# Optimization experiments

Measured on AMD Instinct MI355X. Metric: run time of the kernel, lower is better.

## Reference

```python
import jax, jax.numpy as jnp
import numpy as np

LATENT = 256
HEADS = 4
DIM_HEAD = 256            # dim_head = latent_channels
INNER = HEADS * DIM_HEAD  # 1024
ROT_DIM = DIM_HEAD // 2   # rotary dim per coordinate (relative_emb_dim=2)
MIN_FREQ = 1.0 / 64.0     # 1/res
ROT_SCALE = 16.0          # CrossFormer scale
FF_SCALE = 0.5            # Gaussian Fourier feature scale
PI = 3.141592653589793
OUT_CH = 3


def _gelu(x):
    return jax.nn.gelu(x, approximate=False)  # torch nn.GELU default (erf)


def _rot_freqs(coords, dim):
    # coords: [b, n] -> freqs [b, n, dim]
    inv_freq = 1.0 / (10000.0 ** (jnp.arange(0, dim, 2, dtype=jnp.float32) / dim))
    t = coords * (ROT_SCALE / MIN_FREQ)
    f = t[..., None] * inv_freq               # [b, n, dim//2]
    return jnp.concatenate([f, f], axis=-1)    # [b, n, dim]


def _rotate_half(x):
    x1, x2 = jnp.split(x, 2, axis=-1)
    return jnp.concatenate([-x2, x1], axis=-1)


def _apply_rot(t, freqs):
    return t * jnp.cos(freqs) + _rotate_half(t) * jnp.sin(freqs)


def _apply_2d_rot(t, fx, fy):
    d = t.shape[-1]
    tx, ty = t[..., : d // 2], t[..., d // 2 :]
    return jnp.concatenate([_apply_rot(tx, fx), _apply_rot(ty, fy)], axis=-1)


def _inst_norm(t, eps=1e-5):
    # galerkin normalization: non-affine norm over head dim (InstanceNorm1d, affine=False)
    mu = jnp.mean(t, axis=-1, keepdims=True)
    var = jnp.var(t, axis=-1, keepdims=True)
    return (t - mu) * jax.lax.rsqrt(var + eps)


def setup_inputs() -> dict:
    key = jax.random.key(0)
    ks = jax.random.split(key, 20)
    b, nq, nc = 8, 4096, 4096
    s = 0.02
    return {
        "z": jax.random.normal(ks[0], (b, nc, LATENT), jnp.float32),
        "query_pos": jax.random.uniform(ks[1], (b, nq, 2), jnp.float32),
        "context_pos": jax.random.uniform(ks[2], (b, nc, 2), jnp.float32),
        # GaussianFourierFeatureTransform buffer B: [2, mapping_size=latent/2]
        "B_ff": jax.random.normal(ks[3], (2, LATENT // 2), jnp.float32) * FF_SCALE,
        # coordinate_projection linears (bias=False)
        "Wc1": jax.random.normal(ks[4], (LATENT, LATENT), jnp.float32) * s,
        "Wc2": jax.random.normal(ks[5], (LATENT, LATENT), jnp.float32) * s,
        # cross attention projections
        "Wq": jax.random.normal(ks[6], (LATENT, INNER), jnp.float32) * s,
        "Wkv": jax.random.normal(ks[7], (LATENT, 2 * INNER), jnp.float32) * s,
        "Wo": jax.random.normal(ks[8], (INNER, LATENT), jnp.float32) * s,
        "bo": jnp.zeros((LATENT,), jnp.float32),
        # feed-forward (mlp_dim = latent)
        "Wf1": jax.random.normal(ks[9], (LATENT, LATENT), jnp.float32) * s,
        "bf1": jnp.zeros((LATENT,), jnp.float32),
        "Wf2": jax.random.normal(ks[10], (LATENT, LATENT), jnp.float32) * s,
        "bf2": jnp.zeros((LATENT,), jnp.float32),
        # output head
        "Wh1": jax.random.normal(ks[11], (LATENT + 2, LATENT), jnp.float32) * s,
        "Wh2": jax.random.normal(ks[12], (LATENT, LATENT // 2), jnp.float32) * s,
        "Wh3": jax.random.normal(ks[13], (LATENT // 2, OUT_CH), jnp.float32) * s,
        "bh3": jnp.zeros((OUT_CH,), jnp.float32),
    }


def reference(z, query_pos, context_pos, B_ff, Wc1, Wc2, Wq, Wkv, Wo, bo,
              Wf1, bf1, Wf2, bf2, Wh1, Wh2, Wh3, bh3):
    b, nq, _ = query_pos.shape
    nc = z.shape[1]
    # 1) Gaussian Fourier features + 2-layer projection
    ff = 2.0 * PI * (query_pos @ B_ff)                           # [b, nq, latent/2]
    x = jnp.concatenate([jnp.sin(ff), jnp.cos(ff)], axis=-1)      # [b, nq, latent]
    x = _gelu(x @ Wc1) @ Wc2
    # 2) galerkin cross attention with 2D rotary relative pos emb
    q = (x @ Wq).reshape(b, nq, HEADS, DIM_HEAD).transpose(0, 2, 1, 3)
    k, v = jnp.split(z @ Wkv, 2, axis=-1)
    k = k.reshape(b, nc, HEADS, DIM_HEAD).transpose(0, 2, 1, 3)
    v = v.reshape(b, nc, HEADS, DIM_HEAD).transpose(0, 2, 1, 3)
    fxq = _rot_freqs(query_pos[..., 0], ROT_DIM)[:, None]         # [b,1,nq,rot]
    fyq = _rot_freqs(query_pos[..., 1], ROT_DIM)[:, None]
    fxk = _rot_freqs(context_pos[..., 0], ROT_DIM)[:, None]
    fyk = _rot_freqs(context_pos[..., 1], ROT_DIM)[:, None]
    q = _apply_2d_rot(q, fxq, fyq)
    k = _apply_2d_rot(k, fxk, fyk)
    k = _inst_norm(k)
    v = _inst_norm(v)
    kv = jnp.einsum('bhnd,bhne->bhde', k, v)                      # [b,h,d,d]
    attn = jnp.einsum('bhmd,bhde->bhme', q, kv) * (1.0 / nc)      # [b,h,nq,d]
    attn = attn.transpose(0, 2, 1, 3).reshape(b, nq, INNER)
    x = (attn @ Wo + bo) + x                                      # residual
    x = (_gelu(x @ Wf1 + bf1) @ Wf2 + bf2) + x                    # FFN residual
    # 3) output head on [features, coords]
    h = jnp.concatenate([x, query_pos], axis=-1)
    h = _gelu(h @ Wh1)
    h = _gelu(h @ Wh2)
    return h @ Wh3 + bh3                                          # [b, nq, out_ch]
```

## Files before the change

### kernel.cpp

```cpp
#include <hip/hip_runtime.h>
#include <math.h>


typedef unsigned short u16;
typedef __attribute__((ext_vector_type(4))) float f32x4;
typedef __attribute__((ext_vector_type(8))) short s16x8;
typedef __attribute__((ext_vector_type(8))) unsigned short u16x8;
typedef __attribute__((ext_vector_type(4))) unsigned short u16x4;

#define LOG2_1E4_D64 0.20762050593046013f

#define VMCNT(n) do{ asm volatile("s_waitcnt vmcnt(" #n ")" ::: "memory"); \
                     __builtin_amdgcn_sched_barrier(0); }while(0)
#define BARRIER() do{ __builtin_amdgcn_s_barrier(); \
                      __builtin_amdgcn_sched_barrier(0); }while(0)

__device__ __forceinline__ u16 f2b(float f){
  union { float f; unsigned u; } v; v.f = f;
  unsigned u = v.u;
  u += 0x7FFFu + ((u >> 16) & 1u);
  return (u16)(u >> 16);
}
__device__ __forceinline__ float b2f(u16 b){
  union { unsigned u; float f; } v; v.u = ((unsigned)b) << 16; return v.f;
}
__device__ __forceinline__ float gelu_f(float x){
  return 0.5f * x * (1.0f + erff(x * 0.7071067811865475f));
}

#if __has_builtin(__builtin_amdgcn_global_load_lds)
#define HAVE_GLL 1
typedef const __attribute__((address_space(1))) void* as1cv;
typedef __attribute__((address_space(3))) void* as3v;
__device__ __forceinline__ void gload16(const void* g, void* l){
  __builtin_amdgcn_global_load_lds((as1cv)g, (as3v)l, 16, 0, 0);
}
#else
#define HAVE_GLL 0
#endif


struct PrepArgs {
  const float* z; u16* Zb;
  const float* qp; const float* Bff; u16* X0;
  const float* W[9]; u16* Wt[9];
  int K[9]; int N[9]; int boff[10];
  int castB, tcB;
};
__global__ __launch_bounds__(256) void k_prep(PrepArgs a){
  int b = blockIdx.x, tid = threadIdx.x;
  if (b < a.castB){
    long i = (long)b * 256 + tid;
    float4 f = ((const float4*)a.z)[i];
    u16x4 o = { f2b(f.x), f2b(f.y), f2b(f.z), f2b(f.w) };
    ((u16x4*)a.Zb)[i] = o;
  } else if (b < a.castB + a.tcB){
    int bb = b - a.castB;
    int w = 0;
    while (bb >= a.boff[w+1]) w++;
    int idx = (bb - a.boff[w]) * 256 + tid;
    int K = a.K[w], N = a.N[w];
    int n = idx / K, k = idx - n * K;
    a.Wt[w][idx] = f2b(a.W[w][(long)k * N + n]);
  } else {
    int bb = b - a.castB - a.tcB;
    long r = (long)bb * 2 + (tid >> 7);
    int j = tid & 127;
    float qx = a.qp[r*2], qy = a.qp[r*2+1];
    float ff = 6.283185307179586f * (qx * a.Bff[j] + qy * a.Bff[128 + j]);
    a.X0[r*256 + j]       = f2b(sinf(ff));
    a.X0[r*256 + 128 + j] = f2b(cosf(ff));
  }
}

__global__ __launch_bounds__(256) void k_red(const float* __restrict__ p, u16* __restrict__ out, long stride){
  long i = (long)blockIdx.x * 256 + threadIdx.x;
  f32x4 s = ((const f32x4*)p)[i];
  s += ((const f32x4*)(p + stride))[i];
  s += ((const f32x4*)(p + 2*stride))[i];
  s += ((const f32x4*)(p + 3*stride))[i];
  u16x4 o = { f2b(s[0]), f2b(s[1]), f2b(s[2]), f2b(s[3]) };
  ((u16x4*)out)[i] = o;
}

__global__ __launch_bounds__(256) void k_final(const u16* __restrict__ H2, const float* __restrict__ Wh3,
                                               const float* __restrict__ bh3, float* __restrict__ out){
  long r = (long)blockIdx.x * 256 + threadIdx.x;
  float a0 = bh3[0], a1 = bh3[1], a2 = bh3[2];
  const u16x8* hrow = (const u16x8*)(H2 + r*128);
#pragma unroll
  for (int c8 = 0; c8 < 16; c8++){
    u16x8 hv = hrow[c8];
#pragma unroll
    for (int e = 0; e < 8; e++){
      float f = b2f(hv[e]);
      int k = c8*8 + e;
      a0 += f * Wh3[k*3];
      a1 += f * Wh3[k*3+1];
      a2 += f * Wh3[k*3+2];
    }
  }
  out[r*3] = a0; out[r*3+1] = a1; out[r*3+2] = a2;
}


template<int MODE>
__global__ __launch_bounds__(256, 2)
void gemm_fuse(const u16* __restrict__ A, const u16* __restrict__ Bw,
               u16* __restrict__ outK, u16* __restrict__ outV,
               const float* __restrict__ pos){
  __shared__ char smem[49152];
  u16* AsB = (u16*)smem;
  u16* BsB = (u16*)(smem + 16384);

  int tid  = threadIdx.x;
  int lane = tid & 63;
  int wave = tid >> 6;
  int wm = (wave & 1) << 6;
  int wn = (wave >> 1) << 7;
  int whalf = wave >> 1;
  int yb = blockIdx.x;
  int h  = yb & 3;
  bool isK = (MODE == 1) || (yb < 4);
  long m0 = (long)blockIdx.y * 128;

  int r15 = lane & 15;
  int cc  = lane >> 4;
  int fsw = (cc ^ ((r15 >> 1) & 3)) * 8;
  const u16* Bh = Bw + (long)yb * 65536;

  f32x4 acc[4][8];
#pragma unroll
  for (int i = 0; i < 4; i++)
#pragma unroll
    for (int j = 0; j < 8; j++)
      acc[i][j] = f32x4{0.f, 0.f, 0.f, 0.f};

#if HAVE_GLL
  int srow  = lane >> 2;
  int scolS = ((lane & 3) ^ ((lane >> 3) & 3)) * 8;
  int aRow[2], bRow[4];
  const u16 *gA[2], *gB[4];
#pragma unroll
  for (int t = 0; t < 2; t++){
    aRow[t] = (wave*2 + t) * 16;
    gA[t] = A + (m0 + aRow[t] + srow) * 256 + scolS;
  }
#pragma unroll
  for (int t = 0; t < 4; t++){
    bRow[t] = (wave*4 + t) * 16;
    gB[t] = Bh + (bRow[t] + srow) * 256 + scolS;
  }
  auto stage = [&](int buf, int kk){
    u16* ab = AsB + buf*4096;
    u16* bb = BsB + buf*8192;
#pragma unroll
    for (int t = 0; t < 2; t++) gload16(gA[t] + kk*32, ab + aRow[t]*32);
#pragma unroll
    for (int t = 0; t < 4; t++) gload16(gB[t] + kk*32, bb + bRow[t]*32);
  };
  auto compute = [&](int buf){
    const u16* ab = AsB + buf*4096;
    const u16* bb = BsB + buf*8192;
    s16x8 af[4], bf[8];
#pragma unroll
    for (int i = 0; i < 4; i++) af[i] = *(const s16x8*)&ab[(wm + i*16 + r15)*32 + fsw];
#pragma unroll
    for (int j = 0; j < 8; j++) bf[j] = *(const s16x8*)&bb[(wn + j*16 + r15)*32 + fsw];
#pragma unroll
    for (int i = 0; i < 4; i++)
#pragma unroll
      for (int j = 0; j < 8; j++)
        acc[i][j] = __builtin_amdgcn_mfma_f32_16x16x32_bf16(af[i], bf[j], acc[i][j], 0, 0, 0);
  };

  stage(0, 0);
  stage(1, 1);
  int cur = 0;
  for (int t = 0; t < 7; t++){
    VMCNT(6);
    BARRIER();
    compute(cur);
    __builtin_amdgcn_sched_barrier(0);
    BARRIER();
    if (t + 2 < 8) stage(cur, t + 2);
    cur ^= 1;
  }
  VMCNT(0);
  BARRIER();
  compute(cur);
#else
  int sm = tid >> 2, sc = tid & 3;
  for (int k0 = 0; k0 < 256; k0 += 32){
    u16x8 va  = *(const u16x8*)(A + (m0 + sm)*256 + sc*8 + k0);
    u16x8 va1 = *(const u16x8*)(A + (m0 + sm + 64)*256 + sc*8 + k0);
    u16x8 vb0 = *(const u16x8*)(Bh + (sm      )*256 + sc*8 + k0);
    u16x8 vb1 = *(const u16x8*)(Bh + (sm + 64 )*256 + sc*8 + k0);
    u16x8 vb2 = *(const u16x8*)(Bh + (sm + 128)*256 + sc*8 + k0);
    u16x8 vb3 = *(const u16x8*)(Bh + (sm + 192)*256 + sc*8 + k0);
    __syncthreads();
    *(u16x8*)&AsB[sm*32 + sc*8] = va;
    *(u16x8*)&AsB[(sm+64)*32 + sc*8] = va1;
    *(u16x8*)&BsB[sm*32 + sc*8] = vb0;
    *(u16x8*)&BsB[(sm+64)*32 + sc*8] = vb1;
    *(u16x8*)&BsB[(sm+128)*32 + sc*8] = vb2;
    *(u16x8*)&BsB[(sm+192)*32 + sc*8] = vb3;
    __syncthreads();
    s16x8 af[4], bf[8];
#pragma unroll
    for (int i = 0; i < 4; i++) af[i] = *(const s16x8*)&AsB[(wm + i*16 + r15)*32 + cc*8];
#pragma unroll
    for (int j = 0; j < 8; j++) bf[j] = *(const s16x8*)&BsB[(wn + j*16 + r15)*32 + cc*8];
#pragma unroll
    for (int i = 0; i < 4; i++)
#pragma unroll
      for (int j = 0; j < 8; j++)
        acc[i][j] = __builtin_amdgcn_mfma_f32_16x16x32_bf16(af[i], bf[j], acc[i][j], 0, 0, 0);
    __syncthreads();
  }
#endif

  if (isK){
    float invf4[4];
#pragma unroll
    for (int jl = 0; jl < 4; jl++)
      invf4[jl] = 1024.0f * exp2f(-(float)(jl*16 + r15) * LOG2_1E4_D64);
#pragma unroll
    for (int i = 0; i < 4; i++){
#pragma unroll
      for (int r = 0; r < 4; r++){
        long n = m0 + wm + i*16 + cc*4 + r;
        float p = pos[n*2 + whalf];
#pragma unroll
        for (int jl = 0; jl < 4; jl++){
          float a = p * invf4[jl];
          float s = __sinf(a), c = __cosf(a);
          float t0 = acc[i][jl][r], t1 = acc[i][jl+4][r];
          acc[i][jl][r]   = t0*c - t1*s;
          acc[i][jl+4][r] = t1*c + t0*s;
        }
      }
    }
  }

  if constexpr (MODE == 1){
#pragma unroll
    for (int i = 0; i < 4; i++)
#pragma unroll
      for (int j = 0; j < 8; j++)
#pragma unroll
        for (int r = 0; r < 4; r++){
          long row = m0 + wm + i*16 + cc*4 + r;
          int col = yb*256 + wn + j*16 + r15;
          outK[row*1024 + col] = f2b(acc[i][j][r]);
        }
  } else {
    u16*   TB  = (u16*)smem;
    float* PS1 = (float*)(smem + 32768);
    float* PS2 = (float*)(smem + 33792);

    __syncthreads();

#pragma unroll
    for (int i = 0; i < 4; i++){
#pragma unroll
      for (int r = 0; r < 4; r++){
        float s1 = 0.f, s2 = 0.f;
#pragma unroll
        for (int j = 0; j < 8; j++){
          float v = acc[i][j][r];
          s1 += v; s2 += v*v;
        }
#pragma unroll
        for (int m = 1; m < 16; m <<= 1){
          s1 += __shfl_xor(s1, m, 64);
          s2 += __shfl_xor(s2, m, 64);
        }
        int rowid = (wave&1)*64 + i*16 + cc*4 + r;
        if (r15 == 0){ PS1[whalf*128 + rowid] = s1; PS2[whalf*128 + rowid] = s2; }
      }
    }
    __syncthreads();
#pragma unroll
    for (int i = 0; i < 4; i++){
#pragma unroll
      for (int r = 0; r < 4; r++){
        int rowid = (wave&1)*64 + i*16 + cc*4 + r;
        float s1 = PS1[rowid] + PS1[128 + rowid];
        float s2 = PS2[rowid] + PS2[128 + rowid];
        float mu  = s1 * 0.00390625f;
        float var = s2 * 0.00390625f - mu*mu;
        float inv = 1.0f / sqrtf(var + 1e-5f);
#pragma unroll
        for (int j = 0; j < 8; j++)
          acc[i][j][r] = (acc[i][j][r] - mu) * inv;
      }
    }
    __syncthreads();

    u16* outp = isK ? outK : outV;
    int bb  = (int)(m0 >> 12);
    int nn0 = (int)(m0 & 4095);
    long matbase = ((long)(bb*4 + h) * 256) * 4096;
#pragma unroll
    for (int p = 0; p < 2; p++){
      if ((wave & 1) == p){
#pragma unroll
        for (int i = 0; i < 4; i++)
#pragma unroll
          for (int j = 0; j < 8; j++)
#pragma unroll
            for (int r = 0; r < 4; r++){
              int nl = i*16 + cc*4 + r;
              int d  = wn + j*16 + r15;
              TB[nl*256 + (d ^ ((nl>>2)<<1))] = f2b(acc[i][j][r]);
            }
      }
      __syncthreads();
      {
        int n4 = (lane & 15) * 4;
        int sw = (lane & 15) << 1;
#pragma unroll
        for (int rnd = 0; rnd < 16; rnd++){
          int d = rnd*16 + wave*4 + (lane >> 4);
          u16x4 vv;
#pragma unroll
          for (int jj = 0; jj < 4; jj++) vv[jj] = TB[(n4+jj)*256 + (d ^ sw)];
          *(u16x4*)(outp + matbase + (long)d*4096 + nn0 + p*64 + n4) = vv;
        }
      }
      __syncthreads();
    }
  }
}


enum { EP_B = 0, EP_GELU = 1, EP_BIAS_GELU = 2, EP_BIAS_RESB = 3, EP_SCALE = 4,
       EP_QP_GELU = 5, EP_F32 = 6 };

struct GArgs {
  const u16* A; const u16* B;
  u16* Cb; float* Cf;
  const float* bias; const u16* res; const float* qp; const float* wtail;
  float scale;
  int M, N, K, lda, ldb, ldc, NLO;
  long sAh, sAl, sBh, sBl, sCh, sCl;
};

template<int EP>
__global__ __launch_bounds__(256, 2)
void gemm_k(GArgs g){
  int z = blockIdx.z;
  int zh = z / g.NLO, zl = z - zh * g.NLO;
  const u16* A = g.A + (long)zh * g.sAh + (long)zl * g.sAl;
  const u16* B = g.B + (long)zh * g.sBh + (long)zl * g.sBl;
  long coff = (long)zh * g.sCh + (long)zl * g.sCl;

  __shared__ u16 As[2][128*32];
  __shared__ u16 Bs[2][128*32];

  int tid  = threadIdx.x;
  int lane = tid & 63;
  int wave = tid >> 6;
  int wm = (wave & 1) << 6;
  int wn = (wave >> 1) << 6;
  long m0 = (long)blockIdx.x * 128;
  long n0 = (long)blockIdx.y * 128;

  int r15 = lane & 15;
  int cc  = lane >> 4;
  int fsw = (cc ^ ((r15 >> 1) & 3)) * 8;

  f32x4 acc[4][4];
#pragma unroll
  for (int i = 0; i < 4; i++)
#pragma unroll
    for (int j = 0; j < 4; j++)
      acc[i][j] = f32x4{0.f, 0.f, 0.f, 0.f};

#if HAVE_GLL
  int srow  = lane >> 2;
  int scolS = ((lane & 3) ^ ((lane >> 3) & 3)) * 8;
  int aRow[2];
  const u16 *gA[2], *gB[2];
#pragma unroll
  for (int t = 0; t < 2; t++){
    aRow[t] = (wave*2 + t) * 16;
    gA[t] = A + (m0 + aRow[t] + srow) * g.lda + scolS;
    gB[t] = B + (n0 + aRow[t] + srow) * g.ldb + scolS;
  }
  auto stage = [&](int buf, int kk){
#pragma unroll
    for (int t = 0; t < 2; t++){
      gload16(gA[t] + kk*32, &As[buf][aRow[t]*32]);
      gload16(gB[t] + kk*32, &Bs[buf][aRow[t]*32]);
    }
  };
  auto compute = [&](int buf){
    s16x8 af[4], bf[4];
#pragma unroll
    for (int i = 0; i < 4; i++) af[i] = *(const s16x8*)&As[buf][(wm + i*16 + r15)*32 + fsw];
#pragma unroll
    for (int i = 0; i < 4; i++) bf[i] = *(const s16x8*)&Bs[buf][(wn + i*16 + r15)*32 + fsw];
#pragma unroll
    for (int i = 0; i < 4; i++)
#pragma unroll
      for (int j = 0; j < 4; j++)
        acc[i][j] = __builtin_amdgcn_mfma_f32_16x16x32_bf16(af[i], bf[j], acc[i][j], 0, 0, 0);
  };

  int nt = g.K >> 5;
  stage(0, 0);
  stage(1, 1);
  int cur = 0;
  for (int t = 0; t < nt - 1; t++){
    VMCNT(4);
    BARRIER();
    compute(cur);
    __builtin_amdgcn_sched_barrier(0);
    BARRIER();
    if (t + 2 < nt) stage(cur, t + 2);
    cur ^= 1;
  }
  VMCNT(0);
  BARRIER();
  compute(cur);
#else
  int sm  = tid >> 2;
  int sc  = tid & 3;
  for (int k0 = 0; k0 < g.K; k0 += 32){
    u16x8 va0 = *(const u16x8*)(A + (m0 + sm )*g.lda + sc*8 + k0);
    u16x8 va1 = *(const u16x8*)(A + (m0 + sm + 64)*g.lda + sc*8 + k0);
    u16x8 vb0 = *(const u16x8*)(B + (n0 + sm )*g.ldb + sc*8 + k0);
    u16x8 vb1 = *(const u16x8*)(B + (n0 + sm + 64)*g.ldb + sc*8 + k0);
    __syncthreads();
    *(u16x8*)&As[0][sm*32 + sc*8] = va0;
    *(u16x8*)&As[0][(sm+64)*32 + sc*8] = va1;
    *(u16x8*)&Bs[0][sm*32 + sc*8] = vb0;
    *(u16x8*)&Bs[0][(sm+64)*32 + sc*8] = vb1;
    __syncthreads();
    s16x8 af[4], bf[4];
#pragma unroll
    for (int i = 0; i < 4; i++) af[i] = *(const s16x8*)&As[0][(wm + i*16 + r15)*32 + cc*8];
#pragma unroll
    for (int i = 0; i < 4; i++) bf[i] = *(const s16x8*)&Bs[0][(wn + i*16 + r15)*32 + cc*8];
#pragma unroll
    for (int i = 0; i < 4; i++)
#pragma unroll
      for (int j = 0; j < 4; j++)
        acc[i][j] = __builtin_amdgcn_mfma_f32_16x16x32_bf16(af[i], bf[j], acc[i][j], 0, 0, 0);
    __syncthreads();
  }
#endif

  int colb = (int)n0 + wn + r15;
  int rowb = (int)m0 + wm + cc * 4;
#pragma unroll
  for (int i = 0; i < 4; i++){
#pragma unroll
    for (int j = 0; j < 4; j++){
      int col = colb + j*16;
#pragma unroll
      for (int r = 0; r < 4; r++){
        int row = rowb + i*16 + r;
        float v = acc[i][j][r];
        if constexpr (EP == EP_B){
          g.Cb[coff + (long)row * g.ldc + col] = f2b(v);
        } else if constexpr (EP == EP_GELU){
          g.Cb[coff + (long)row * g.ldc + col] = f2b(gelu_f(v));
        } else if constexpr (EP == EP_BIAS_GELU){
          v = gelu_f(v + g.bias[col]);
          g.Cb[coff + (long)row * g.ldc + col] = f2b(v);
        } else if constexpr (EP == EP_BIAS_RESB){
          v += g.bias[col] + b2f(g.res[(long)row * g.ldc + col]);
          g.Cb[coff + (long)row * g.ldc + col] = f2b(v);
        } else if constexpr (EP == EP_SCALE){
          g.Cb[coff + (long)row * g.ldc + col] = f2b(v * g.scale);
        } else if constexpr (EP == EP_F32){
          g.Cf[coff + (long)row * g.ldc + col] = v;
        } else {
          v += g.qp[(long)row*2] * g.wtail[col] + g.qp[(long)row*2+1] * g.wtail[256+col];
          g.Cb[coff + (long)row * g.ldc + col] = f2b(gelu_f(v));
        }
      }
    }
  }
}


extern "C" void kernel_launch(void* const* d_in, const int* in_sizes, int n_in,
                              void* d_out, int out_size, void* d_ws, size_t ws_size,
                              hipStream_t stream){
  const float* z   = (const float*)d_in[0];
  const float* qp  = (const float*)d_in[1];
  const float* cp  = (const float*)d_in[2];
  const float* Bff = (const float*)d_in[3];
  const float* Wc1 = (const float*)d_in[4];
  const float* Wc2 = (const float*)d_in[5];
  const float* Wq  = (const float*)d_in[6];
  const float* Wkv = (const float*)d_in[7];
  const float* Wo  = (const float*)d_in[8];
  const float* bo  = (const float*)d_in[9];
  const float* Wf1 = (const float*)d_in[10];
  const float* bf1 = (const float*)d_in[11];
  const float* Wf2 = (const float*)d_in[12];
  const float* bf2 = (const float*)d_in[13];
  const float* Wh1 = (const float*)d_in[14];
  const float* Wh2 = (const float*)d_in[15];
  const float* Wh3 = (const float*)d_in[16];
  const float* bh3 = (const float*)d_in[17];
  float* out = (float*)d_out;
  (void)in_sizes; (void)n_in; (void)out_size;

  size_t mb = ws_size >> 20;
  int C;
  if      (mb >= 264) C = 1;
  else if (mb >= 168) C = 2;
  else if (mb >= 120) C = 4;
  else                C = 8;
  const int NB = 8 / C;
  const long R = (long)NB * 4096;

  char* ws = (char*)d_ws;
  const size_t MB = 1024*1024;
  u16* WqT  = (u16*)(ws + 0);
  u16* WkvT = (u16*)(ws + 512*1024);
  u16* WoT  = (u16*)(ws + 1536*1024);
  u16* Wc1T = (u16*)(ws + 2048*1024);
  u16* Wc2T = (u16*)(ws + (2048+128)*1024);
  u16* Wf1T = (u16*)(ws + (2048+256)*1024);
  u16* Wf2T = (u16*)(ws + (2048+384)*1024);
  u16* Wh1T = (u16*)(ws + (2048+512)*1024);
  u16* Wh2T = (u16*)(ws + (2048+640)*1024);
  u16* R1 = (u16*)(ws + 4*MB);
  u16* R2 = (u16*)(ws + 20*MB);
  u16* R3 = (u16*)(ws + 36*MB);
  u16* R4 = (u16*)(ws + 52*MB);
  u16* kvT = (u16*)(ws + 68*MB);
  u16* BIG1 = (u16*)(ws + 72*MB);
  u16* BIG2 = (u16*)((char*)BIG1 + (size_t)NB*8*MB);
  u16* BIG3 = (u16*)((char*)BIG2 + (size_t)NB*8*MB);

  u16* X0b = R1; u16* X2b = R1;
  u16* Tb  = R2; u16* H1b = R2;
  u16* Xb  = R3;
  u16* Zb  = R4; u16* H2b = R4;

  auto G = [&](int ep, const u16* A, const u16* B, u16* Cb, float* Cf,
               const float* bias, const u16* res, const float* qq, const float* wtail,
               float scale, int M, int N, int K, int lda, int ldb, int ldc,
               int nz, int NLO, long sAh, long sAl, long sBh, long sBl, long sCh, long sCl){
    GArgs g;
    g.A=A; g.B=B; g.Cb=Cb; g.Cf=Cf; g.bias=bias; g.res=res; g.qp=qq; g.wtail=wtail;
    g.scale=scale; g.M=M; g.N=N; g.K=K; g.lda=lda; g.ldb=ldb; g.ldc=ldc; g.NLO=NLO;
    g.sAh=sAh; g.sAl=sAl; g.sBh=sBh; g.sBl=sBl; g.sCh=sCh; g.sCl=sCl;
    dim3 gr(M/128, N/128, nz); dim3 bl(256);
    switch(ep){
      case EP_B:          gemm_k<EP_B><<<gr,bl,0,stream>>>(g); break;
      case EP_GELU:       gemm_k<EP_GELU><<<gr,bl,0,stream>>>(g); break;
      case EP_BIAS_GELU:  gemm_k<EP_BIAS_GELU><<<gr,bl,0,stream>>>(g); break;
      case EP_BIAS_RESB:  gemm_k<EP_BIAS_RESB><<<gr,bl,0,stream>>>(g); break;
      case EP_SCALE:      gemm_k<EP_SCALE><<<gr,bl,0,stream>>>(g); break;
      case EP_QP_GELU:    gemm_k<EP_QP_GELU><<<gr,bl,0,stream>>>(g); break;
      case EP_F32:        gemm_k<EP_F32><<<gr,bl,0,stream>>>(g); break;
    }
  };

  {
    PrepArgs a;
    a.z = z; a.Zb = Zb; a.qp = qp; a.Bff = Bff; a.X0 = X0b;
    const float* Ws[9] = { Wq, Wkv, Wo, Wc1, Wc2, Wf1, Wf2, Wh1, Wh2 };
    u16* Wts[9] = { WqT, WkvT, WoT, Wc1T, Wc2T, Wf1T, Wf2T, Wh1T, Wh2T };
    int Ks[9] = { 256, 256, 1024, 256, 256, 256, 256, 256, 256 };
    int Ns[9] = { 1024, 2048, 256, 256, 256, 256, 256, 256, 128 };
    int off = 0;
    for (int i = 0; i < 9; i++){
      a.W[i] = Ws[i]; a.Wt[i] = Wts[i]; a.K[i] = Ks[i]; a.N[i] = Ns[i];
      a.boff[i] = off; off += Ks[i]*Ns[i]/256;
    }
    a.boff[9] = off;
    a.castB = 8192; a.tcB = off;
    k_prep<<<dim3(8192 + off + 16384), dim3(256), 0, stream>>>(a);
  }

  G(EP_GELU, X0b, Wc1T, Tb, 0, 0,0,0,0, 1.f, 32768,256,256, 256,256,256, 1,1, 0,0,0,0,0,0);
  G(EP_B,    Tb,  Wc2T, Xb, 0, 0,0,0,0, 1.f, 32768,256,256, 256,256,256, 1,1, 0,0,0,0,0,0);

  for (int c = 0; c < C; c++){
    long row0 = (long)c * R;
    const u16* Zc = Zb + row0 * 256;
    gemm_fuse<0><<<dim3(8, (int)(R/128)), dim3(256), 0, stream>>>(Zc, WkvT, BIG2, BIG3, cp + row0*2);
    G(EP_F32, BIG3, BIG2, 0, (float*)BIG1, 0,0,0,0, 1.f,
      256,256,1024, 4096,4096,256, 4*NB*4, NB*4,
      1024,1048576, 1024,1048576, (long)NB*4*65536,65536);
    k_red<<<dim3(NB*256), dim3(256), 0, stream>>>((float*)BIG1, kvT + (long)c*NB*4*65536, (long)NB*4*65536);
    gemm_fuse<1><<<dim3(4, (int)(R/128)), dim3(256), 0, stream>>>(Xb + row0*256, WqT, BIG1, 0, qp + row0*2);
    G(EP_SCALE, BIG1, kvT + (long)c*NB*4*65536, BIG2, 0, 0,0,0,0, 1.0f/4096.0f,
      4096,256,256, 1024,256,1024, NB*4,4, 4194304,256, 262144,65536, 4194304,256);
    G(EP_BIAS_RESB, BIG2, WoT, X2b + row0*256, 0, bo, Xb + row0*256, 0,0, 1.f,
      (int)R,256,1024, 1024,1024,256, 1,1, 0,0,0,0,0,0);
  }

  G(EP_BIAS_GELU, X2b, Wf1T, Tb, 0, bf1, 0,0,0, 1.f, 32768,256,256, 256,256,256, 1,1, 0,0,0,0,0,0);
  G(EP_BIAS_RESB, Tb, Wf2T, Xb, 0, bf2, X2b, 0,0, 1.f, 32768,256,256, 256,256,256, 1,1, 0,0,0,0,0,0);
  G(EP_QP_GELU, Xb, Wh1T, H1b, 0, 0,0, qp, Wh1 + 65536, 1.f, 32768,256,256, 256,256,256, 1,1, 0,0,0,0,0,0);
  G(EP_GELU, H1b, Wh2T, H2b, 0, 0,0,0,0, 1.f, 32768,128,256, 256,256,128, 1,1, 0,0,0,0,0,0);
  k_final<<<dim3(128), dim3(256), 0, stream>>>(H2b, Wh3, bh3, out);
}
```

Measured before the change: 526.6 us.

## Load GEMM MFMA fragments directly from global memory, dropping LDS staging

Both GEMM kernels stop staging A/B tiles through double-buffered LDS with global_load_lds and barriers. Each wave now loads its MFMA fragments straight from global memory, relying on cache for reuse. The generic GEMM's launch bound is raised to 4 blocks per CU to get more occupancy for hiding latency. The cost is that tiles shared between waves are fetched repeatedly from L1/L2 instead of once into LDS, and the explicit prefetch pipeline is gone.

```diff
diff --git a/kernel.cpp b/kernel.cpp
--- a/kernel.cpp
+++ b/kernel.cpp
@@ -10,11 +10,6 @@
 
 #define LOG2_1E4_D64 0.20762050593046013f
 
-#define VMCNT(n) do{ asm volatile("s_waitcnt vmcnt(" #n ")" ::: "memory"); \
-                     __builtin_amdgcn_sched_barrier(0); }while(0)
-#define BARRIER() do{ __builtin_amdgcn_s_barrier(); \
-                      __builtin_amdgcn_sched_barrier(0); }while(0)
-
 __device__ __forceinline__ u16 f2b(float f){
   union { float f; unsigned u; } v; v.f = f;
   unsigned u = v.u;
@@ -27,17 +22,6 @@
 __device__ __forceinline__ float gelu_f(float x){
   return 0.5f * x * (1.0f + erff(x * 0.7071067811865475f));
 }
-
-#if __has_builtin(__builtin_amdgcn_global_load_lds)
-#define HAVE_GLL 1
-typedef const __attribute__((address_space(1))) void* as1cv;
-typedef __attribute__((address_space(3))) void* as3v;
-__device__ __forceinline__ void gload16(const void* g, void* l){
-  __builtin_amdgcn_global_load_lds((as1cv)g, (as3v)l, 16, 0, 0);
-}
-#else
-#define HAVE_GLL 0
-#endif
 
 
 struct PrepArgs {
@@ -109,10 +93,6 @@
 void gemm_fuse(const u16* __restrict__ A, const u16* __restrict__ Bw,
                u16* __restrict__ outK, u16* __restrict__ outV,
                const float* __restrict__ pos){
-  __shared__ char smem[49152];
-  u16* AsB = (u16*)smem;
-  u16* BsB = (u16*)(smem + 16384);
-
   int tid  = threadIdx.x;
   int lane = tid & 63;
   int wave = tid >> 6;
@@ -126,8 +106,10 @@
 
   int r15 = lane & 15;
   int cc  = lane >> 4;
-  int fsw = (cc ^ ((r15 >> 1) & 3)) * 8;
   const u16* Bh = Bw + (long)yb * 65536;
+
+  const u16* pA = A + (m0 + wm + r15) * 256 + cc*8;
+  const u16* pB = Bh + (wn + r15) * 256 + cc*8;
 
   f32x4 acc[4][8];
 #pragma unroll
@@ -136,89 +118,19 @@
     for (int j = 0; j < 8; j++)
       acc[i][j] = f32x4{0.f, 0.f, 0.f, 0.f};
 
-#if HAVE_GLL
-  int srow  = lane >> 2;
-  int scolS = ((lane & 3) ^ ((lane >> 3) & 3)) * 8;
-  int aRow[2], bRow[4];
-  const u16 *gA[2], *gB[4];
-#pragma unroll
-  for (int t = 0; t < 2; t++){
-    aRow[t] = (wave*2 + t) * 16;
-    gA[t] = A + (m0 + aRow[t] + srow) * 256 + scolS;
-  }
-#pragma unroll
-  for (int t = 0; t < 4; t++){
-    bRow[t] = (wave*4 + t) * 16;
-    gB[t] = Bh + (bRow[t] + srow) * 256 + scolS;
-  }
-  auto stage = [&](int buf, int kk){
-    u16* ab = AsB + buf*4096;
-    u16* bb = BsB + buf*8192;
-#pragma unroll
-    for (int t = 0; t < 2; t++) gload16(gA[t] + kk*32, ab + aRow[t]*32);
-#pragma unroll
-    for (int t = 0; t < 4; t++) gload16(gB[t] + kk*32, bb + bRow[t]*32);
-  };
-  auto compute = [&](int buf){
-    const u16* ab = AsB + buf*4096;
-    const u16* bb = BsB + buf*8192;
+#pragma unroll 4
+  for (int k0 = 0; k0 < 256; k0 += 32){
     s16x8 af[4], bf[8];
 #pragma unroll
-    for (int i = 0; i < 4; i++) af[i] = *(const s16x8*)&ab[(wm + i*16 + r15)*32 + fsw];
-#pragma unroll
-    for (int j = 0; j < 8; j++) bf[j] = *(const s16x8*)&bb[(wn + j*16 + r15)*32 + fsw];
+    for (int i = 0; i < 4; i++) af[i] = *(const s16x8*)(pA + i*16*256 + k0);
+#pragma unroll
+    for (int j = 0; j < 8; j++) bf[j] = *(const s16x8*)(pB + j*16*256 + k0);
 #pragma unroll
     for (int i = 0; i < 4; i++)
 #pragma unroll
       for (int j = 0; j < 8; j++)
         acc[i][j] = __builtin_amdgcn_mfma_f32_16x16x32_bf16(af[i], bf[j], acc[i][j], 0, 0, 0);
-  };
-
-  stage(0, 0);
-  stage(1, 1);
-  int cur = 0;
-  for (int t = 0; t < 7; t++){
-    VMCNT(6);
-    BARRIER();
-    compute(cur);
-    __builtin_amdgcn_sched_barrier(0);
-    BARRIER();
-    if (t + 2 < 8) stage(cur, t + 2);
-    cur ^= 1;
-  }
-  VMCNT(0);
-  BARRIER();
-  compute(cur);
-#else
-  int sm = tid >> 2, sc = tid & 3;
-  for (int k0 = 0; k0 < 256; k0 += 32){
-    u16x8 va  = *(const u16x8*)(A + (m0 + sm)*256 + sc*8 + k0);
-    u16x8 va1 = *(const u16x8*)(A + (m0 + sm + 64)*256 + sc*8 + k0);
-    u16x8 vb0 = *(const u16x8*)(Bh + (sm      )*256 + sc*8 + k0);
-    u16x8 vb1 = *(const u16x8*)(Bh + (sm + 64 )*256 + sc*8 + k0);
-    u16x8 vb2 = *(const u16x8*)(Bh + (sm + 128)*256 + sc*8 + k0);
-    u16x8 vb3 = *(const u16x8*)(Bh + (sm + 192)*256 + sc*8 + k0);
-    __syncthreads();
-    *(u16x8*)&AsB[sm*32 + sc*8] = va;
-    *(u16x8*)&AsB[(sm+64)*32 + sc*8] = va1;
-    *(u16x8*)&BsB[sm*32 + sc*8] = vb0;
-    *(u16x8*)&BsB[(sm+64)*32 + sc*8] = vb1;
-    *(u16x8*)&BsB[(sm+128)*32 + sc*8] = vb2;
-    *(u16x8*)&BsB[(sm+192)*32 + sc*8] = vb3;
-    __syncthreads();
-    s16x8 af[4], bf[8];
-#pragma unroll
-    for (int i = 0; i < 4; i++) af[i] = *(const s16x8*)&AsB[(wm + i*16 + r15)*32 + cc*8];
-#pragma unroll
-    for (int j = 0; j < 8; j++) bf[j] = *(const s16x8*)&BsB[(wn + j*16 + r15)*32 + cc*8];
-#pragma unroll
-    for (int i = 0; i < 4; i++)
-#pragma unroll
-      for (int j = 0; j < 8; j++)
-        acc[i][j] = __builtin_amdgcn_mfma_f32_16x16x32_bf16(af[i], bf[j], acc[i][j], 0, 0, 0);
-    __syncthreads();
-  }
-#endif
+  }
 
   if (isK){
     float invf4[4];
@@ -255,11 +167,9 @@
           outK[row*1024 + col] = f2b(acc[i][j][r]);
         }
   } else {
-    u16*   TB  = (u16*)smem;
-    float* PS1 = (float*)(smem + 32768);
-    float* PS2 = (float*)(smem + 33792);
-
-    __syncthreads();
+    __shared__ u16  TB[64*256];
+    __shared__ float PS1[2][128];
+    __shared__ float PS2[2][128];
 
 #pragma unroll
     for (int i = 0; i < 4; i++){
@@ -277,7 +187,7 @@
           s2 += __shfl_xor(s2, m, 64);
         }
         int rowid = (wave&1)*64 + i*16 + cc*4 + r;
-        if (r15 == 0){ PS1[whalf*128 + rowid] = s1; PS2[whalf*128 + rowid] = s2; }
+        if (r15 == 0){ PS1[whalf][rowid] = s1; PS2[whalf][rowid] = s2; }
       }
     }
     __syncthreads();
@@ -286,8 +196,8 @@
 #pragma unroll
       for (int r = 0; r < 4; r++){
         int rowid = (wave&1)*64 + i*16 + cc*4 + r;
-        float s1 = PS1[rowid] + PS1[128 + rowid];
-        float s2 = PS2[rowid] + PS2[128 + rowid];
+        float s1 = PS1[0][rowid] + PS1[1][rowid];
+        float s2 = PS2[0][rowid] + PS2[1][rowid];
         float mu  = s1 * 0.00390625f;
         float var = s2 * 0.00390625f - mu*mu;
         float inv = 1.0f / sqrtf(var + 1e-5f);
@@ -348,16 +258,13 @@
 };
 
 template<int EP>
-__global__ __launch_bounds__(256, 2)
+__global__ __launch_bounds__(256, 4)
 void gemm_k(GArgs g){
   int z = blockIdx.z;
   int zh = z / g.NLO, zl = z - zh * g.NLO;
   const u16* A = g.A + (long)zh * g.sAh + (long)zl * g.sAl;
   const u16* B = g.B + (long)zh * g.sBh + (long)zl * g.sBl;
   long coff = (long)zh * g.sCh + (long)zl * g.sCl;
-
-  __shared__ u16 As[2][128*32];
-  __shared__ u16 Bs[2][128*32];
 
   int tid  = threadIdx.x;
   int lane = tid & 63;
@@ -369,7 +276,10 @@
 
   int r15 = lane & 15;
   int cc  = lane >> 4;
-  int fsw = (cc ^ ((r15 >> 1) & 3)) * 8;
+  int lda = g.lda, ldb = g.ldb;
+
+  const u16* pA = A + (m0 + wm + r15) * lda + cc*8;
+  const u16* pB = B + (n0 + wn + r15) * ldb + cc*8;
 
   f32x4 acc[4][4];
 #pragma unroll
@@ -378,80 +288,19 @@
     for (int j = 0; j < 4; j++)
       acc[i][j] = f32x4{0.f, 0.f, 0.f, 0.f};
 
-#if HAVE_GLL
-  int srow  = lane >> 2;
-  int scolS = ((lane & 3) ^ ((lane >> 3) & 3)) * 8;
-  int aRow[2];
-  const u16 *gA[2], *gB[2];
-#pragma unroll
-  for (int t = 0; t < 2; t++){
-    aRow[t] = (wave*2 + t) * 16;
-    gA[t] = A + (m0 + aRow[t] + srow) * g.lda + scolS;
-    gB[t] = B + (n0 + aRow[t] + srow) * g.ldb + scolS;
-  }
-  auto stage = [&](int buf, int kk){
-#pragma unroll
-    for (int t = 0; t < 2; t++){
-      gload16(gA[t] + kk*32, &As[buf][aRow[t]*32]);
-      gload16(gB[t] + kk*32, &Bs[buf][aRow[t]*32]);
-    }
-  };
-  auto compute = [&](int buf){
+#pragma unroll 4
+  for (int k0 = 0; k0 < g.K; k0 += 32){
     s16x8 af[4], bf[4];
 #pragma unroll
-    for (int i = 0; i < 4; i++) af[i] = *(const s16x8*)&As[buf][(wm + i*16 + r15)*32 + fsw];
-#pragma unroll
-    for (int i = 0; i < 4; i++) bf[i] = *(const s16x8*)&Bs[buf][(wn + i*16 + r15)*32 + fsw];
+    for (int i = 0; i < 4; i++) af[i] = *(const s16x8*)(pA + i*16*lda + k0);
+#pragma unroll
+    for (int j = 0; j < 4; j++) bf[j] = *(const s16x8*)(pB + j*16*ldb + k0);
 #pragma unroll
     for (int i = 0; i < 4; i++)
 #pragma unroll
       for (int j = 0; j < 4; j++)
         acc[i][j] = __builtin_amdgcn_mfma_f32_16x16x32_bf16(af[i], bf[j], acc[i][j], 0, 0, 0);
-  };
-
-  int nt = g.K >> 5;
-  stage(0, 0);
-  stage(1, 1);
-  int cur = 0;
-  for (int t = 0; t < nt - 1; t++){
-    VMCNT(4);
-    BARRIER();
-    compute(cur);
-    __builtin_amdgcn_sched_barrier(0);
-    BARRIER();
-    if (t + 2 < nt) stage(cur, t + 2);
-    cur ^= 1;
-  }
-  VMCNT(0);
-  BARRIER();
-  compute(cur);
-#else
-  int sm  = tid >> 2;
-  int sc  = tid & 3;
-  for (int k0 = 0; k0 < g.K; k0 += 32){
-    u16x8 va0 = *(const u16x8*)(A + (m0 + sm )*g.lda + sc*8 + k0);
-    u16x8 va1 = *(const u16x8*)(A + (m0 + sm + 64)*g.lda + sc*8 + k0);
-    u16x8 vb0 = *(const u16x8*)(B + (n0 + sm )*g.ldb + sc*8 + k0);
-    u16x8 vb1 = *(const u16x8*)(B + (n0 + sm + 64)*g.ldb + sc*8 + k0);
-    __syncthreads();
-    *(u16x8*)&As[0][sm*32 + sc*8] = va0;
-    *(u16x8*)&As[0][(sm+64)*32 + sc*8] = va1;
-    *(u16x8*)&Bs[0][sm*32 + sc*8] = vb0;
-    *(u16x8*)&Bs[0][(sm+64)*32 + sc*8] = vb1;
-    __syncthreads();
-    s16x8 af[4], bf[4];
-#pragma unroll
-    for (int i = 0; i < 4; i++) af[i] = *(const s16x8*)&As[0][(wm + i*16 + r15)*32 + cc*8];
-#pragma unroll
-    for (int i = 0; i < 4; i++) bf[i] = *(const s16x8*)&Bs[0][(wn + i*16 + r15)*32 + cc*8];
-#pragma unroll
-    for (int i = 0; i < 4; i++)
-#pragma unroll
-      for (int j = 0; j < 4; j++)
-        acc[i][j] = __builtin_amdgcn_mfma_f32_16x16x32_bf16(af[i], bf[j], acc[i][j], 0, 0, 0);
-    __syncthreads();
-  }
-#endif
+  }
 
   int colb = (int)n0 + wn + r15;
   int rowb = (int)m0 + wm + cc * 4;
```

Measured after the change: 775.1 us. +47.2%, slower.

## Stage MODE 1 gemm_fuse output through swizzled LDS and raise occupancy hint

Applied to the files above, without the earlier changes.

The MODE 1 epilogue of gemm_fuse used to write each bf16 result element straight to global memory in a scattered pattern. It now stages each 64-row half of the tile in shared memory with an XOR swizzle, then writes full rows with 16-byte vector stores. Separately, the launch-bounds minimum blocks per CU rises from 2 to 3 for both gemm_fuse and gemm_k. That tighter register budget may cause spills, and the staged epilogue adds extra barriers.

```diff
diff --git a/kernel.cpp b/kernel.cpp
--- a/kernel.cpp
+++ b/kernel.cpp
@@ -105,7 +105,7 @@
 
 
 template<int MODE>
-__global__ __launch_bounds__(256, 2)
+__global__ __launch_bounds__(256, 3)
 void gemm_fuse(const u16* __restrict__ A, const u16* __restrict__ Bw,
                u16* __restrict__ outK, u16* __restrict__ outV,
                const float* __restrict__ pos){
@@ -244,16 +244,42 @@
   }
 
   if constexpr (MODE == 1){
-#pragma unroll
-    for (int i = 0; i < 4; i++)
-#pragma unroll
-      for (int j = 0; j < 8; j++)
-#pragma unroll
-        for (int r = 0; r < 4; r++){
-          long row = m0 + wm + i*16 + cc*4 + r;
-          int col = yb*256 + wn + j*16 + r15;
-          outK[row*1024 + col] = f2b(acc[i][j][r]);
+    u16* TB = (u16*)smem;
+    __syncthreads();
+    long rowg = m0;
+#pragma unroll
+    for (int p = 0; p < 2; p++){
+      if ((wave & 1) == p){
+#pragma unroll
+        for (int i = 0; i < 4; i++)
+#pragma unroll
+          for (int j = 0; j < 8; j++)
+#pragma unroll
+            for (int r = 0; r < 4; r++){
+              int nl = i*16 + cc*4 + r;
+              int d  = wn + j*16 + r15;
+              TB[nl*256 + (d ^ ((nl>>2)<<1))] = f2b(acc[i][j][r]);
+            }
+      }
+      __syncthreads();
+      {
+        int nl = tid >> 2;
+        int cb = (tid & 3) * 8;
+        int sw = (nl >> 2) << 1;
+        int swHi = sw & ~7, swLo = sw & 7;
+        u16* orow = outK + (rowg + p*64 + nl) * 1024 + yb*256;
+#pragma unroll
+        for (int c8 = 0; c8 < 8; c8++){
+          int cblk = cb + c8*32;
+          u16x8 vv = *(const u16x8*)&TB[nl*256 + (cblk ^ swHi)];
+          u16x8 ov;
+#pragma unroll
+          for (int e = 0; e < 8; e++) ov[e] = vv[e ^ swLo];
+          *(u16x8*)(orow + cblk) = ov;
         }
+      }
+      __syncthreads();
+    }
   } else {
     u16*   TB  = (u16*)smem;
     float* PS1 = (float*)(smem + 32768);
@@ -348,7 +374,7 @@
 };
 
 template<int EP>
-__global__ __launch_bounds__(256, 2)
+__global__ __launch_bounds__(256, 3)
 void gemm_k(GArgs g){
   int z = blockIdx.z;
   int zh = z / g.NLO, zl = z - zh * g.NLO;
```

After: 1.140 ms. 2.17x slower.
